# Kernel tuning notes

Measured on AMD Instinct MI355X. Metric: run time of the kernel, lower is better.

## Reference

```python
import jax, jax.numpy as jnp
import numpy as np

EMB = 1024
HEADS = 16


def setup_inputs() -> dict:
    key = jax.random.key(0)
    ks = jax.random.split(key, 9)
    s = 1.0 / np.sqrt(EMB)
    x = jax.random.normal(ks[0], (2, 2048, EMB), dtype=jnp.float32)
    Wq = jax.random.normal(ks[1], (EMB, EMB), dtype=jnp.float32) * s
    bq = jnp.zeros((EMB,), dtype=jnp.float32)
    Wk = jax.random.normal(ks[2], (EMB, EMB), dtype=jnp.float32) * s
    bk = jnp.zeros((EMB,), dtype=jnp.float32)
    Wv = jax.random.normal(ks[3], (EMB, EMB), dtype=jnp.float32) * s
    bv = jnp.zeros((EMB,), dtype=jnp.float32)
    Wo = jax.random.normal(ks[4], (EMB, EMB), dtype=jnp.float32) * s
    bo = jnp.zeros((EMB,), dtype=jnp.float32)
    return {"x": x, "Wq": Wq, "bq": bq, "Wk": Wk, "bk": bk,
            "Wv": Wv, "bv": bv, "Wo": Wo, "bo": bo}


def reference(x, Wq, bq, Wk, bk, Wv, bv, Wo, bo):
    b, n, e = x.shape
    h = HEADS
    d = e // h
    # q/k/v projections -> [b, h, n, d]
    def split_heads(t):
        return t.reshape(b, n, h, d).transpose(0, 2, 1, 3)
    q = split_heads(x @ Wq.T + bq)
    k = split_heads(x @ Wk.T + bk)
    v = split_heads(x @ Wv.T + bv)
    # NOTE: original scales by sqrt(emb_size), not sqrt(head_dim)
    scaling = jnp.sqrt(jnp.float32(e))
    energy = jnp.einsum('bhqd,bhkd->bhqk', q, k)  # [b,h,n,n]
    att = jax.nn.softmax(energy / scaling, axis=-1)
    out = jnp.einsum('bhqk,bhkd->bhqd', att, v)
    out = out.transpose(0, 2, 1, 3).reshape(b, n, e)
    return out @ Wo.T + bo
```

## Files before the change

### kernel.cpp

```cpp
#include <hip/hip_runtime.h>


typedef short short8  __attribute__((ext_vector_type(8)));
typedef float floatx4 __attribute__((ext_vector_type(4)));

#define SEQ   2048
#define BATCH 2
#define NH    16
#define HD    64
#define EMB   1024

#define QSCALE 0.045084220027780106f

__device__ __forceinline__ unsigned short f32_bf16(float f) {
    unsigned int u = __float_as_uint(f);
    u += 0x7FFF + ((u >> 16) & 1);
    return (unsigned short)(u >> 16);
}

__device__ __forceinline__ unsigned int pk_bf16(float lo, float hi) {
    return __builtin_amdgcn_perm(__float_as_uint(hi) + 0x8000u,
                                 __float_as_uint(lo) + 0x8000u, 0x07060302u);
}

__device__ __forceinline__ void gl_lds16(const unsigned short* g,
                                         unsigned short* l) {
    __builtin_amdgcn_global_load_lds(
        (const __attribute__((address_space(1))) unsigned int*)g,
        (__attribute__((address_space(3))) unsigned int*)l, 16, 0, 0);
}

__global__ __launch_bounds__(256) void convert_all(
        const float* __restrict__ x,  const float* __restrict__ wq,
        const float* __restrict__ wk, const float* __restrict__ wv,
        const float* __restrict__ wo, unsigned short* __restrict__ dst) {
    int i = (blockIdx.x * 256 + threadIdx.x) * 4;
    const float* src; int off;
    if      (i < 4194304) { src = x;  off = 0; }
    else if (i < 5242880) { src = wq; off = 4194304; }
    else if (i < 6291456) { src = wk; off = 5242880; }
    else if (i < 7340032) { src = wv; off = 6291456; }
    else                  { src = wo; off = 7340032; }
    float4 v = *(const float4*)(src + (i - off));
    uint2 o;
    o.x = pk_bf16(v.x, v.y);
    o.y = pk_bf16(v.z, v.w);
    *(uint2*)(dst + i) = o;
}

template <int MODE>
__device__ __forceinline__ void gemm_bt_core(
        unsigned short (* __restrict__ sA)[64],
        unsigned short (* __restrict__ sB)[64],
        const unsigned short* __restrict__ A,
        const unsigned short* __restrict__ B,
        const float* __restrict__ bias,
        unsigned short* __restrict__ outb) {
    const int t    = threadIdx.x;
    const int wave = t >> 6, lane = t & 63;
    const int l15  = lane & 15, quad = lane >> 4;
    const int wm   = (wave >> 1) * 64, wn = (wave & 1) * 64;
    const int m0   = blockIdx.y * 128,  n0 = blockIdx.x * 128;
    const int srow = lane >> 3;
    const int sch  = ((lane & 7) ^ srow) * 8;

    floatx4 acc[4][4] = {};

    for (int k0 = 0; k0 < EMB; k0 += 64) {
        for (int i = 0; i < 4; ++i) {
            int rr  = wave * 32 + i * 8;
            int row = rr + srow;
            gl_lds16(&A[(size_t)(m0 + row) * EMB + k0 + sch], &sA[0][0] + rr * 64);
            gl_lds16(&B[(size_t)(n0 + row) * EMB + k0 + sch], &sB[0][0] + rr * 64);
        }
        __syncthreads();
        for (int ks = 0; ks < 2; ++ks) {
            const int ch = (((ks * 4) + quad) ^ (l15 & 7)) * 8;
            short8 af[4], bf[4];
            for (int i = 0; i < 4; ++i)
                af[i] = *(const short8*)&sA[wm + i * 16 + l15][ch];
            for (int j = 0; j < 4; ++j)
                bf[j] = *(const short8*)&sB[wn + j * 16 + l15][ch];
            for (int i = 0; i < 4; ++i)
                for (int j = 0; j < 4; ++j)
                    acc[i][j] = __builtin_amdgcn_mfma_f32_16x16x32_bf16(
                        af[i], bf[j], acc[i][j], 0, 0, 0);
        }
        __syncthreads();
    }
    if (MODE == 2) {
        for (int i = 0; i < 4; ++i) {
            int row = m0 + wm + i * 16 + quad * 4;
            int bb  = row >> 11, seq = row & 2047;
            for (int j = 0; j < 4; ++j) {
                int col = n0 + wn + j * 16 + l15;
                float bv = bias[col];
                int vtrow = (bb * 16 + (col >> 6)) * 64 + (col & 63);
                uint2 pk;
                pk.x = pk_bf16(acc[i][j][0] + bv, acc[i][j][1] + bv);
                pk.y = pk_bf16(acc[i][j][2] + bv, acc[i][j][3] + bv);
                *(uint2*)&outb[(size_t)vtrow * SEQ + seq] = pk;
            }
        }
    } else {
        const float sc2 = (MODE == 1) ? QSCALE : 1.0f;
        for (int i = 0; i < 4; ++i) {
            int row = m0 + wm + i * 16 + quad * 4;
            for (int j = 0; j < 4; ++j) {
                int col = n0 + wn + j * 16 + l15;
                float bv = bias[col];
                for (int r = 0; r < 4; ++r) {
                    float v = (acc[i][j][r] + bv) * sc2;
                    outb[(size_t)(row + r) * EMB + col] = f32_bf16(v);
                }
            }
        }
    }
}

__global__ __launch_bounds__(256, 3) void gemm_qkv(
        const unsigned short* __restrict__ xb,
        const unsigned short* __restrict__ wq,
        const unsigned short* __restrict__ wk,
        const unsigned short* __restrict__ wv,
        const float* __restrict__ bq, const float* __restrict__ bk,
        const float* __restrict__ bv,
        unsigned short* __restrict__ Q, unsigned short* __restrict__ K,
        unsigned short* __restrict__ VT) {
    __shared__ unsigned short sA[128][64];
    __shared__ unsigned short sB[128][64];
    if      (blockIdx.z == 0) gemm_bt_core<1>(sA, sB, xb, wq, bq, Q);
    else if (blockIdx.z == 1) gemm_bt_core<0>(sA, sB, xb, wk, bk, K);
    else                      gemm_bt_core<2>(sA, sB, xb, wv, bv, VT);
}

__global__ __launch_bounds__(256) void gemm_out(
        const unsigned short* __restrict__ A,
        const unsigned short* __restrict__ B,
        const float* __restrict__ bias, float* __restrict__ out) {
    __shared__ unsigned short sA[128][64];
    __shared__ unsigned short sB[64][64];
    const int t    = threadIdx.x;
    const int wave = t >> 6, lane = t & 63;
    const int l15  = lane & 15, quad = lane >> 4;
    const int wm   = wave * 32;
    const int m0   = blockIdx.y * 128,  n0 = blockIdx.x * 64;
    const int srow = lane >> 3;
    const int sch  = ((lane & 7) ^ srow) * 8;

    floatx4 acc[2][4] = {};

    for (int k0 = 0; k0 < EMB; k0 += 64) {
        {
            for (int i = 0; i < 4; ++i) {
                int rr = wave * 32 + i * 8;
                gl_lds16(&A[(size_t)(m0 + rr + srow) * EMB + k0 + sch],
                         &sA[0][0] + rr * 64);
            }
            for (int i = 0; i < 2; ++i) {
                int rr = wave * 16 + i * 8;
                gl_lds16(&B[(size_t)(n0 + rr + srow) * EMB + k0 + sch],
                         &sB[0][0] + rr * 64);
            }
        }
        __syncthreads();
        for (int ks = 0; ks < 2; ++ks) {
            const int ch = (((ks * 4) + quad) ^ (l15 & 7)) * 8;
            short8 af[2], bf[4];
            for (int i = 0; i < 2; ++i)
                af[i] = *(const short8*)&sA[wm + i * 16 + l15][ch];
            for (int j = 0; j < 4; ++j)
                bf[j] = *(const short8*)&sB[j * 16 + l15][ch];
            for (int i = 0; i < 2; ++i)
                for (int j = 0; j < 4; ++j)
                    acc[i][j] = __builtin_amdgcn_mfma_f32_16x16x32_bf16(
                        af[i], bf[j], acc[i][j], 0, 0, 0);
        }
        __syncthreads();
    }
    for (int i = 0; i < 2; ++i) {
        int row = m0 + wm + i * 16 + quad * 4;
        for (int j = 0; j < 4; ++j) {
            int col = n0 + j * 16 + l15;
            float bv = bias[col];
            for (int r = 0; r < 4; ++r)
                out[(size_t)(row + r) * EMB + col] = acc[i][j][r] + bv;
        }
    }
}

__global__ __launch_bounds__(512) void attn(
        const unsigned short* __restrict__ Q,
        const unsigned short* __restrict__ K,
        const unsigned short* __restrict__ VT,
        unsigned short* __restrict__ O) {
    __shared__ __align__(16) unsigned short smem[33792];
    unsigned short (*sK )[64][64] = (unsigned short (*)[64][64])(smem);
    unsigned short (*sVT)[64][64] = (unsigned short (*)[64][64])(smem + 12288);
    unsigned short (*sP )[72]     = (unsigned short (*)[72])(smem + 24576);

    const int t    = threadIdx.x;
    const int wave = t >> 6, lane = t & 63;
    const int qh   = wave >> 1, kh = wave & 1;
    const int l15  = lane & 15, quad = lane >> 4;
    const int bh   = blockIdx.x;
    const int b    = bh >> 4, h = bh & 15;
    const int q0   = blockIdx.y * 128;
    const size_t rowbase = (size_t)b * SEQ;
    const int colbase  = h * HD;
    const size_t vtbase = (size_t)bh * HD * SEQ;
    const int srow = lane >> 3;
    const int sch  = ((lane & 7) ^ srow) * 8;

    short8 qf[2][2];
    for (int g = 0; g < 2; ++g)
        for (int ks = 0; ks < 2; ++ks)
            qf[g][ks] = *(const short8*)
                &Q[(rowbase + q0 + qh * 32 + g * 16 + l15) * EMB
                   + colbase + ks * 32 + quad * 8];

    float l_part[2] = {0.f, 0.f};
    floatx4 o_acc[2][4] = {};

    const int rr  = wave * 8;
    const int row = rr + srow;
    const int kw   = row & 31;
    const int krow = (row & 32) + ((kw >> 2) & 3) * 8 + ((kw >> 4) & 1) * 4
                     + (kw & 3);

    gl_lds16(&K[(rowbase + krow) * EMB + colbase + sch], &sK[0][0][0] + rr * 64);
    gl_lds16(&VT[vtbase + (size_t)row * SEQ + sch],      &sVT[0][0][0] + rr * 64);

    int cur = 0;
    for (int it = 0; it < SEQ / 64; ++it) {
        if (it < SEQ / 64 - 1) {
            int nb = cur + 1; if (nb == 3) nb = 0;
            int kt = (it + 1) * 64;
            gl_lds16(&K[(rowbase + kt + krow) * EMB + colbase + sch],
                     &sK[nb][0][0] + rr * 64);
            gl_lds16(&VT[vtbase + (size_t)row * SEQ + kt + sch],
                     &sVT[nb][0][0] + rr * 64);
            asm volatile("s_waitcnt vmcnt(2)" ::: "memory");
        } else {
            asm volatile("s_waitcnt vmcnt(0)" ::: "memory");
        }
        asm volatile("s_barrier" ::: "memory");

        const unsigned short (*cK)[64]  = sK[cur];
        const unsigned short (*cVT)[64] = sVT[cur];

        floatx4 s[2][2] = {};
        __builtin_amdgcn_s_setprio(1);
        for (int ks = 0; ks < 2; ++ks) {
            const int ch = (((ks * 4) + quad) ^ (l15 & 7)) * 8;
            short8 kf[2];
            for (int m = 0; m < 2; ++m)
                kf[m] = *(const short8*)&cK[kh * 32 + m * 16 + l15][ch];
            for (int g = 0; g < 2; ++g)
                for (int m = 0; m < 2; ++m)
                    s[g][m] = __builtin_amdgcn_mfma_f32_16x16x32_bf16(
                        kf[m], qf[g][ks], s[g][m], 0, 0, 0);
        }
        __builtin_amdgcn_s_setprio(0);

        short8 vf[4];
        {
            const int ch = ((kh * 4 + quad) ^ (l15 & 7)) * 8;
            for (int mi = 0; mi < 4; ++mi)
                vf[mi] = *(const short8*)&cVT[mi * 16 + l15][ch];
        }

        union { uint4 u; short8 s8; } pf[2];
        for (int g = 0; g < 2; ++g) {
            float lp = l_part[g];
            unsigned int w[4];
            for (int m = 0; m < 2; ++m) {
                float p0 = __builtin_amdgcn_exp2f(s[g][m][0]);
                float p1 = __builtin_amdgcn_exp2f(s[g][m][1]);
                float p2 = __builtin_amdgcn_exp2f(s[g][m][2]);
                float p3 = __builtin_amdgcn_exp2f(s[g][m][3]);
                lp += (p0 + p1) + (p2 + p3);
                w[m * 2 + 0] = pk_bf16(p0, p1);
                w[m * 2 + 1] = pk_bf16(p2, p3);
            }
            pf[g].u.x = w[0]; pf[g].u.y = w[1];
            pf[g].u.z = w[2]; pf[g].u.w = w[3];
            l_part[g] = lp;
        }

        __builtin_amdgcn_s_setprio(1);
        for (int g = 0; g < 2; ++g)
            for (int mi = 0; mi < 4; ++mi)
                o_acc[g][mi] = __builtin_amdgcn_mfma_f32_16x16x32_bf16(
                    vf[mi], pf[g].s8, o_acc[g][mi], 0, 0, 0);
        __builtin_amdgcn_s_setprio(0);

        cur = cur + 1; if (cur == 3) cur = 0;
    }

    float la[2];
    for (int g = 0; g < 2; ++g) {
        float v = l_part[g];
        v += __shfl_xor(v, 16, 64);
        v += __shfl_xor(v, 32, 64);
        la[g] = v;
    }

    __syncthreads();
    float* oscr = (float*)smem;
    float* lscr = (float*)smem + 128 * 68;
    if (kh == 1) {
        for (int g = 0; g < 2; ++g) {
            int q = qh * 32 + g * 16 + l15;
            for (int mi = 0; mi < 4; ++mi)
                *(floatx4*)&oscr[q * 68 + mi * 16 + quad * 4] = o_acc[g][mi];
            if (quad == 0) lscr[q] = la[g];
        }
    }
    __syncthreads();
    if (kh == 0) {
        for (int g = 0; g < 2; ++g) {
            int q = qh * 32 + g * 16 + l15;
            const float inv_l = 1.0f / (la[g] + lscr[q]);
            for (int mi = 0; mi < 4; ++mi) {
                floatx4 o1 = *(const floatx4*)&oscr[q * 68 + mi * 16 + quad * 4];
                float c0 = (o_acc[g][mi][0] + o1[0]) * inv_l;
                float c1 = (o_acc[g][mi][1] + o1[1]) * inv_l;
                float c2 = (o_acc[g][mi][2] + o1[2]) * inv_l;
                float c3 = (o_acc[g][mi][3] + o1[3]) * inv_l;
                uint2 pk;
                pk.x = pk_bf16(c0, c1);
                pk.y = pk_bf16(c2, c3);
                *(uint2*)&sP[q][mi * 16 + quad * 4] = pk;
            }
        }
        __builtin_amdgcn_s_waitcnt(0);
        const int ql = lane >> 2, dh = (lane & 3) * 16;
        for (int g = 0; g < 2; ++g) {
            const size_t grow = rowbase + q0 + qh * 32 + g * 16 + ql;
            for (int i = 0; i < 2; ++i) {
                uint4 v = *(const uint4*)&sP[qh * 32 + g * 16 + ql][dh + i * 8];
                *(uint4*)&O[grow * EMB + colbase + dh + i * 8] = v;
            }
        }
    }
}

extern "C" void kernel_launch(void* const* d_in, const int* in_sizes, int n_in,
                              void* d_out, int out_size, void* d_ws, size_t ws_size,
                              hipStream_t stream) {
    const float* x  = (const float*)d_in[0];
    const float* Wq = (const float*)d_in[1];
    const float* bq = (const float*)d_in[2];
    const float* Wk = (const float*)d_in[3];
    const float* bk = (const float*)d_in[4];
    const float* Wv = (const float*)d_in[5];
    const float* bv = (const float*)d_in[6];
    const float* Wo = (const float*)d_in[7];
    const float* bo = (const float*)d_in[8];

    unsigned short* ws  = (unsigned short*)d_ws;
    unsigned short* xb  = ws;
    unsigned short* wqb = ws + 4194304;
    unsigned short* wkb = ws + 5242880;
    unsigned short* wvb = ws + 6291456;
    unsigned short* wob = ws + 7340032;
    unsigned short* Qb  = ws + 8388608;
    unsigned short* Kb  = ws + 12582912;
    unsigned short* VTb = ws + 16777216;
    unsigned short* Ob  = ws + 20971520;

    convert_all<<<8192, 256, 0, stream>>>(x, Wq, Wk, Wv, Wo, ws);
    gemm_qkv<<<dim3(8, 32, 3), 256, 0, stream>>>(xb, wqb, wkb, wvb,
                                                 bq, bk, bv, Qb, Kb, VTb);
    attn<<<dim3(32, 16), 512, 0, stream>>>(Qb, Kb, VTb, Ob);
    gemm_out<<<dim3(16, 32), 256, 0, stream>>>(Ob, wob, bo, (float*)d_out);
}
```

Baseline: 175.1 us.

## Deepen attention K/V prefetch to four stages and software-pipeline QK^T

The attention kernel moves from a 3-slot ring to a 4-slot LDS ring and keeps three K/V tiles in flight. The QK^T MFMAs for tile it+1 are issued in the same iteration as the exp/bf16 pack and PV MFMAs for tile it, so MFMA and transcendental work can interleave and the dependency on the score results is hidden. This costs extra registers for a second score accumulator, which could lower occupancy. The epilogue output staging buffer is moved into the reused LDS region, so total LDS use stays below the old size.

New measurement: 178.6 us. About the same (+2.0%).

```diff
diff --git a/kernel.cpp b/kernel.cpp
--- a/kernel.cpp
+++ b/kernel.cpp
@@ -194,10 +194,9 @@
         const unsigned short* __restrict__ K,
         const unsigned short* __restrict__ VT,
         unsigned short* __restrict__ O) {
-    __shared__ __align__(16) unsigned short smem[33792];
+    __shared__ __align__(16) unsigned short smem[32768];
     unsigned short (*sK )[64][64] = (unsigned short (*)[64][64])(smem);
-    unsigned short (*sVT)[64][64] = (unsigned short (*)[64][64])(smem + 12288);
-    unsigned short (*sP )[72]     = (unsigned short (*)[72])(smem + 24576);
+    unsigned short (*sVT)[64][64] = (unsigned short (*)[64][64])(smem + 16384);
 
     const int t    = threadIdx.x;
     const int wave = t >> 6, lane = t & 63;
@@ -228,28 +227,18 @@
     const int krow = (row & 32) + ((kw >> 2) & 3) * 8 + ((kw >> 4) & 1) * 4
                      + (kw & 3);
 
-    gl_lds16(&K[(rowbase + krow) * EMB + colbase + sch], &sK[0][0][0] + rr * 64);
-    gl_lds16(&VT[vtbase + (size_t)row * SEQ + sch],      &sVT[0][0][0] + rr * 64);
-
-    int cur = 0;
-    for (int it = 0; it < SEQ / 64; ++it) {
-        if (it < SEQ / 64 - 1) {
-            int nb = cur + 1; if (nb == 3) nb = 0;
-            int kt = (it + 1) * 64;
-            gl_lds16(&K[(rowbase + kt + krow) * EMB + colbase + sch],
-                     &sK[nb][0][0] + rr * 64);
-            gl_lds16(&VT[vtbase + (size_t)row * SEQ + kt + sch],
-                     &sVT[nb][0][0] + rr * 64);
-            asm volatile("s_waitcnt vmcnt(2)" ::: "memory");
-        } else {
-            asm volatile("s_waitcnt vmcnt(0)" ::: "memory");
-        }
-        asm volatile("s_barrier" ::: "memory");
-
-        const unsigned short (*cK)[64]  = sK[cur];
-        const unsigned short (*cVT)[64] = sVT[cur];
-
-        floatx4 s[2][2] = {};
+    for (int pt = 0; pt < 3; ++pt) {
+        gl_lds16(&K[(rowbase + pt * 64 + krow) * EMB + colbase + sch],
+                 &sK[pt][0][0] + rr * 64);
+        gl_lds16(&VT[vtbase + (size_t)row * SEQ + pt * 64 + sch],
+                 &sVT[pt][0][0] + rr * 64);
+    }
+    asm volatile("s_waitcnt vmcnt(4)" ::: "memory");
+    asm volatile("s_barrier" ::: "memory");
+
+    floatx4 s_cur[2][2] = {};
+    {
+        const unsigned short (*cK)[64] = sK[0];
         __builtin_amdgcn_s_setprio(1);
         for (int ks = 0; ks < 2; ++ks) {
             const int ch = (((ks * 4) + quad) ^ (l15 & 7)) * 8;
@@ -258,11 +247,43 @@
                 kf[m] = *(const short8*)&cK[kh * 32 + m * 16 + l15][ch];
             for (int g = 0; g < 2; ++g)
                 for (int m = 0; m < 2; ++m)
-                    s[g][m] = __builtin_amdgcn_mfma_f32_16x16x32_bf16(
-                        kf[m], qf[g][ks], s[g][m], 0, 0, 0);
+                    s_cur[g][m] = __builtin_amdgcn_mfma_f32_16x16x32_bf16(
+                        kf[m], qf[g][ks], s_cur[g][m], 0, 0, 0);
         }
         __builtin_amdgcn_s_setprio(0);
-
+    }
+
+    for (int it = 0; it < SEQ / 64; ++it) {
+        if (it < 30) asm volatile("s_waitcnt vmcnt(2)" ::: "memory");
+        else         asm volatile("s_waitcnt vmcnt(0)" ::: "memory");
+        asm volatile("s_barrier" ::: "memory");
+
+        if (it + 3 < SEQ / 64) {
+            int nb = (it + 3) & 3, kt = (it + 3) * 64;
+            gl_lds16(&K[(rowbase + kt + krow) * EMB + colbase + sch],
+                     &sK[nb][0][0] + rr * 64);
+            gl_lds16(&VT[vtbase + (size_t)row * SEQ + kt + sch],
+                     &sVT[nb][0][0] + rr * 64);
+        }
+
+        floatx4 s_next[2][2] = {};
+        if (it + 1 < SEQ / 64) {
+            const unsigned short (*cK)[64] = sK[(it + 1) & 3];
+            __builtin_amdgcn_s_setprio(1);
+            for (int ks = 0; ks < 2; ++ks) {
+                const int ch = (((ks * 4) + quad) ^ (l15 & 7)) * 8;
+                short8 kf[2];
+                for (int m = 0; m < 2; ++m)
+                    kf[m] = *(const short8*)&cK[kh * 32 + m * 16 + l15][ch];
+                for (int g = 0; g < 2; ++g)
+                    for (int m = 0; m < 2; ++m)
+                        s_next[g][m] = __builtin_amdgcn_mfma_f32_16x16x32_bf16(
+                            kf[m], qf[g][ks], s_next[g][m], 0, 0, 0);
+            }
+            __builtin_amdgcn_s_setprio(0);
+        }
+
+        const unsigned short (*cVT)[64] = sVT[it & 3];
         short8 vf[4];
         {
             const int ch = ((kh * 4 + quad) ^ (l15 & 7)) * 8;
@@ -275,10 +296,10 @@
             float lp = l_part[g];
             unsigned int w[4];
             for (int m = 0; m < 2; ++m) {
-                float p0 = __builtin_amdgcn_exp2f(s[g][m][0]);
-                float p1 = __builtin_amdgcn_exp2f(s[g][m][1]);
-                float p2 = __builtin_amdgcn_exp2f(s[g][m][2]);
-                float p3 = __builtin_amdgcn_exp2f(s[g][m][3]);
+                float p0 = __builtin_amdgcn_exp2f(s_cur[g][m][0]);
+                float p1 = __builtin_amdgcn_exp2f(s_cur[g][m][1]);
+                float p2 = __builtin_amdgcn_exp2f(s_cur[g][m][2]);
+                float p3 = __builtin_amdgcn_exp2f(s_cur[g][m][3]);
                 lp += (p0 + p1) + (p2 + p3);
                 w[m * 2 + 0] = pk_bf16(p0, p1);
                 w[m * 2 + 1] = pk_bf16(p2, p3);
@@ -295,7 +316,9 @@
                     vf[mi], pf[g].s8, o_acc[g][mi], 0, 0, 0);
         __builtin_amdgcn_s_setprio(0);
 
-        cur = cur + 1; if (cur == 3) cur = 0;
+        for (int g = 0; g < 2; ++g)
+            for (int m = 0; m < 2; ++m)
+                s_cur[g][m] = s_next[g][m];
     }
 
     float la[2];
@@ -309,6 +332,7 @@
     __syncthreads();
     float* oscr = (float*)smem;
     float* lscr = (float*)smem + 128 * 68;
+    unsigned short (*sPb)[72] = (unsigned short (*)[72])(smem + 18432);
     if (kh == 1) {
         for (int g = 0; g < 2; ++g) {
             int q = qh * 32 + g * 16 + l15;
@@ -331,7 +355,7 @@
                 uint2 pk;
                 pk.x = pk_bf16(c0, c1);
                 pk.y = pk_bf16(c2, c3);
-                *(uint2*)&sP[q][mi * 16 + quad * 4] = pk;
+                *(uint2*)&sPb[q][mi * 16 + quad * 4] = pk;
             }
         }
         __builtin_amdgcn_s_waitcnt(0);
@@ -339,7 +363,7 @@
         for (int g = 0; g < 2; ++g) {
             const size_t grow = rowbase + q0 + qh * 32 + g * 16 + ql;
             for (int i = 0; i < 2; ++i) {
-                uint4 v = *(const uint4*)&sP[qh * 32 + g * 16 + ql][dh + i * 8];
+                uint4 v = *(const uint4*)&sPb[qh * 32 + g * 16 + ql][dh + i * 8];
                 *(uint4*)&O[grow * EMB + colbase + dh + i * 8] = v;
             }
         }
```
